# Optimization experiments

Measured on AMD Instinct MI355X. Metric: run time of the kernel, lower is better.

Reference implementation:

```python
import jax, jax.numpy as jnp
import numpy as np

D_MODEL = 256
N_HEADS = 8
N_LEVELS = 4
N_POINTS = 4
D_FFN = 1024
DH = D_MODEL // N_HEADS
SPATIAL = [(100, 100), (50, 50), (25, 25), (13, 13)]  # (H_l, W_l) per level


def setup_inputs() -> dict:
    key = jax.random.key(0)
    ks = iter(jax.random.split(key, 40))
    N, Lq = 8, 900
    Lin = sum(h * w for h, w in SPATIAL)
    p = lambda shape: jax.random.normal(next(ks), shape, jnp.float32) * 0.02
    inp = {
        'idx': 0,
        'tgt': jax.random.normal(next(ks), (N, Lq, D_MODEL), jnp.float32),
        'query_pos': jax.random.normal(next(ks), (N, Lq, D_MODEL), jnp.float32),
        'reference_points_def': jax.random.uniform(next(ks), (N, Lq, N_LEVELS, 2), jnp.float32),
        'src': jax.random.normal(next(ks), (N, Lin, D_MODEL), jnp.float32),
        'src_spatial_shapes': jnp.array(SPATIAL, jnp.int32),
        'level_start_index': jnp.array(np.cumsum([0] + [h * w for h, w in SPATIAL])[:-1], jnp.int32),
        'src_padding_mask': jnp.zeros((N, Lin), bool),
        # self-attn params
        'wq': p((D_MODEL, D_MODEL)), 'bq': jnp.zeros((D_MODEL,)),
        'wk': p((D_MODEL, D_MODEL)), 'bk': jnp.zeros((D_MODEL,)),
        'wv': p((D_MODEL, D_MODEL)), 'bv': jnp.zeros((D_MODEL,)),
        'wo': p((D_MODEL, D_MODEL)), 'bo': jnp.zeros((D_MODEL,)),
        # MSDeformAttn params
        'w_val': p((D_MODEL, D_MODEL)), 'b_val': jnp.zeros((D_MODEL,)),
        'w_off': p((D_MODEL, N_HEADS * N_LEVELS * N_POINTS * 2)), 'b_off': p((N_HEADS * N_LEVELS * N_POINTS * 2,)),
        'w_att': p((D_MODEL, N_HEADS * N_LEVELS * N_POINTS)), 'b_att': jnp.zeros((N_HEADS * N_LEVELS * N_POINTS,)),
        'w_out': p((D_MODEL, D_MODEL)), 'b_out': jnp.zeros((D_MODEL,)),
        # layer norms
        'ln1_g': jnp.ones((D_MODEL,)), 'ln1_b': jnp.zeros((D_MODEL,)),
        'ln2_g': jnp.ones((D_MODEL,)), 'ln2_b': jnp.zeros((D_MODEL,)),
        'ln3_g': jnp.ones((D_MODEL,)), 'ln3_b': jnp.zeros((D_MODEL,)),
        # FFN
        'w1': p((D_MODEL, D_FFN)), 'b1': jnp.zeros((D_FFN,)),
        'w2': p((D_FFN, D_MODEL)), 'b2': jnp.zeros((D_MODEL,)),
    }
    return inp


def _ln(x, g, b):
    m = x.mean(-1, keepdims=True)
    v = jnp.var(x, axis=-1, keepdims=True)
    return (x - m) / jnp.sqrt(v + 1e-5) * g + b


def _mha(q, k, v, wq, bq, wk, bk, wv, bv, wo, bo):
    N, Lq, _ = q.shape
    split = lambda x: x.reshape(N, -1, N_HEADS, DH).transpose(0, 2, 1, 3)  # (N,H,L,dh)
    qh = split(q @ wq + bq) * (1.0 / np.sqrt(DH))
    kh = split(k @ wk + bk)
    vh = split(v @ wv + bv)
    attn = jax.nn.softmax(jnp.einsum('bhqd,bhkd->bhqk', qh, kh), axis=-1)
    o = jnp.einsum('bhqk,bhkd->bhqd', attn, vh).transpose(0, 2, 1, 3).reshape(N, Lq, D_MODEL)
    return o @ wo + bo


def _bilinear(vflat, Hl, Wl, loc):
    # vflat: (N, H, Hl*Wl, dh); loc: (N, Lq, H, P, 2) normalized (x, y) in [0,1]
    N, Lq, _, P, _ = loc.shape
    x = loc[..., 0] * Wl - 0.5  # align_corners=False pixel coords
    y = loc[..., 1] * Hl - 0.5
    x0 = jnp.floor(x); y0 = jnp.floor(y)
    fx = (x - x0).transpose(0, 2, 1, 3).reshape(N, N_HEADS, Lq * P, 1)
    fy = (y - y0).transpose(0, 2, 1, 3).reshape(N, N_HEADS, Lq * P, 1)
    x0i = x0.astype(jnp.int32); y0i = y0.astype(jnp.int32)

    def gather(xi, yi):
        valid = ((xi >= 0) & (xi < Wl) & (yi >= 0) & (yi < Hl)).astype(vflat.dtype)
        idx = jnp.clip(yi, 0, Hl - 1) * Wl + jnp.clip(xi, 0, Wl - 1)
        idx = idx.transpose(0, 2, 1, 3).reshape(N, N_HEADS, Lq * P)
        g = jnp.take_along_axis(vflat, idx[..., None], axis=2)  # (N,H,Lq*P,dh)
        return g * valid.transpose(0, 2, 1, 3).reshape(N, N_HEADS, Lq * P, 1)

    v = (gather(x0i, y0i) * (1 - fx) * (1 - fy)
         + gather(x0i + 1, y0i) * fx * (1 - fy)
         + gather(x0i, y0i + 1) * (1 - fx) * fy
         + gather(x0i + 1, y0i + 1) * fx * fy)
    return v.reshape(N, N_HEADS, Lq, P, DH)


def _msdeform(query, ref, src, ss, pad_mask, w_val, b_val, w_off, b_off, w_att, b_att, w_out, b_out):
    N, Lq, _ = query.shape
    value = src @ w_val + b_val
    value = jnp.where(pad_mask[..., None], 0.0, value)  # masked_fill on padded memory
    off = (query @ w_off + b_off).reshape(N, Lq, N_HEADS, N_LEVELS, N_POINTS, 2)
    att = jax.nn.softmax((query @ w_att + b_att).reshape(N, Lq, N_HEADS, N_LEVELS * N_POINTS), axis=-1)
    att = att.reshape(N, Lq, N_HEADS, N_LEVELS, N_POINTS)
    normalizer = jnp.array([[w, h] for h, w in ss], jnp.float32)  # (L, 2) as (W_l, H_l)
    loc = ref[:, :, None, :, None, :] + off / normalizer[None, None, None, :, None, :]
    out = jnp.zeros((N, N_HEADS, Lq, DH), value.dtype)
    start = 0
    for l, (Hl, Wl) in enumerate(ss):
        vflat = value[:, start:start + Hl * Wl].reshape(N, Hl * Wl, N_HEADS, DH).transpose(0, 2, 1, 3)
        samp = _bilinear(vflat, Hl, Wl, loc[:, :, :, l])  # (N,H,Lq,P,dh)
        w_l = att[:, :, :, l].transpose(0, 2, 1, 3)  # (N,H,Lq,P)
        out = out + (samp * w_l[..., None]).sum(3)
        start += Hl * Wl
    out = out.transpose(0, 2, 1, 3).reshape(N, Lq, D_MODEL)
    return out @ w_out + b_out, loc


def reference(idx, tgt, query_pos, reference_points_def, src, src_spatial_shapes, level_start_index,
              src_padding_mask, wq, bq, wk, bk, wv, bv, wo, bo,
              w_val, b_val, w_off, b_off, w_att, b_att, w_out, b_out,
              ln1_g, ln1_b, ln2_g, ln2_b, ln3_g, ln3_b, w1, b1, w2, b2):
    ss = [tuple(int(v) for v in row) for row in np.asarray(src_spatial_shapes)]
    # self-attention (is_contrastive=False path)
    q = tgt + query_pos
    tgt2 = _mha(q, q, tgt, wq, bq, wk, bk, wv, bv, wo, bo)
    tgt = _ln(tgt + tgt2, ln2_g, ln2_b)
    # multiscale deformable cross-attention
    tgt2, _ = _msdeform(tgt + query_pos, reference_points_def, src, ss, src_padding_mask,
                        w_val, b_val, w_off, b_off, w_att, b_att, w_out, b_out)
    tgt = _ln(tgt + tgt2, ln1_g, ln1_b)
    # FFN
    tgt2 = jax.nn.relu(tgt @ w1 + b1) @ w2 + b2
    tgt = _ln(tgt + tgt2, ln3_g, ln3_b)
    return tgt
```

## Files before the change

kernel.cpp:

```cpp
#include <hip/hip_runtime.h>
#include <math.h>

#define NB 8
#define LQ 900
#define DM 256
#define NH 8
#define DH 32
#define NL 4
#define NP 4
#define DFFN 1024
#define LIN 13294
#define NVAL (NB*LIN)
#define MROW (NB*LQ)
#define GVAL2 3324

#define WP_VAL 0
#define WP_Q   65536
#define WP_K   131072
#define WP_V   196608
#define WP_O   262144
#define WP_OFF 327680
#define WP_ATT 393216
#define WP_OUT 425984
#define WP_W1  491520
#define WP_W2  753664
#define WP_TOT 1015808

typedef __attribute__((ext_vector_type(8))) short bf16x8;
typedef __attribute__((ext_vector_type(4))) float f32x4;

__device__ __forceinline__ unsigned short f2bf(float x) {
  unsigned u = __float_as_uint(x);
  u += 0x7FFFu + ((u >> 16) & 1u);
  return (unsigned short)(u >> 16);
}

__global__ __launch_bounds__(256) void pack_all(
    const float* __restrict__ w_val, const float* __restrict__ wq,
    const float* __restrict__ wk, const float* __restrict__ wv,
    const float* __restrict__ wo, const float* __restrict__ w_off,
    const float* __restrict__ w_att, const float* __restrict__ w_out,
    const float* __restrict__ w1, const float* __restrict__ w2,
    unsigned short* __restrict__ Wp) {
  const int idx = blockIdx.x * 256 + threadIdx.x;
  const float* src; int r, logN;
  if (idx < WP_Q)        { src = w_val; r = idx;          logN = 8; }
  else if (idx < WP_K)   { src = wq;    r = idx - WP_Q;   logN = 8; }
  else if (idx < WP_V)   { src = wk;    r = idx - WP_K;   logN = 8; }
  else if (idx < WP_O)   { src = wv;    r = idx - WP_V;   logN = 8; }
  else if (idx < WP_OFF) { src = wo;    r = idx - WP_O;   logN = 8; }
  else if (idx < WP_ATT) { src = w_off; r = idx - WP_OFF; logN = 8; }
  else if (idx < WP_OUT) { src = w_att; r = idx - WP_ATT; logN = 7; }
  else if (idx < WP_W1)  { src = w_out; r = idx - WP_OUT; logN = 8; }
  else if (idx < WP_W2)  { src = w1;    r = idx - WP_W1;  logN = 10; }
  else                   { src = w2;    r = idx - WP_W2;  logN = 8; }
  const int N = 1 << logN;
  const int e = r & 7, cs = (r >> 3) & 3;
  const int n = (r >> 5) & (N - 1);
  const int kt = r >> (5 + logN);
  const int c = cs ^ ((n >> 1) & 3);
  const int k = kt * 32 + c * 8 + e;
  Wp[idx] = f2bf(src[(size_t)k * N + n]);
}

__global__ __launch_bounds__(256) void value_gemm2(const float* __restrict__ A,
                                                   const unsigned short* __restrict__ Wp,
                                                   const float* __restrict__ bias,
                                                   unsigned short* __restrict__ C,
                                                   int M) {
  __shared__ char lds[17408];
  short* As = (short*)lds;
  short* Bs = (short*)(lds + 4096);
  const int tid = threadIdx.x;
  const int lane = tid & 63, w = tid >> 6;
  const int wr = w >> 1, wc = w & 1;
  const int l15 = lane & 15, lc = lane >> 4;
  const int nwg = gridDim.x;
  const int qq = nwg >> 3, rr = nwg & 7;
  const int xcd = blockIdx.x & 7, pos = blockIdx.x >> 3;
  const int wgid = (xcd < rr ? xcd * (qq + 1) : rr * (qq + 1) + (xcd - rr) * qq) + pos;
  const int m0 = (wgid >> 1) * 64, n0 = (wgid & 1) * 128;
  const int ar = tid >> 2, ac = tid & 3;
  f32x4 acc[2][4] = {};
  for (int kt = 0; kt < 8; kt++) {
    const int arow = min(m0 + ar, M - 1);
    const float* ap = A + (size_t)arow * 256 + kt * 32 + ac * 8;
    const float4 a0 = ((const float4*)ap)[0], a1 = ((const float4*)ap)[1];
    const unsigned short* bp = Wp + ((size_t)(kt * 256 + n0)) * 32 + tid * 16;
    const uint4 b0 = ((const uint4*)bp)[0], b1 = ((const uint4*)bp)[1];
    __syncthreads();
    {
      bf16x8 av;
      av[0] = (short)f2bf(a0.x); av[1] = (short)f2bf(a0.y);
      av[2] = (short)f2bf(a0.z); av[3] = (short)f2bf(a0.w);
      av[4] = (short)f2bf(a1.x); av[5] = (short)f2bf(a1.y);
      av[6] = (short)f2bf(a1.z); av[7] = (short)f2bf(a1.w);
      *(bf16x8*)&As[ar * 32 + ((ac ^ ((ar >> 1) & 3)) << 3)] = av;
      *(uint4*)&Bs[tid * 16] = b0;
      *(uint4*)&Bs[tid * 16 + 8] = b1;
    }
    __syncthreads();
    bf16x8 af[2], bq[4];
#pragma unroll
    for (int i = 0; i < 2; i++) {
      const int row = wr * 32 + i * 16 + l15;
      af[i] = *(const bf16x8*)&As[row * 32 + ((lc ^ ((row >> 1) & 3)) << 3)];
    }
#pragma unroll
    for (int q = 0; q < 4; q++) {
      const int col = wc * 64 + q * 16 + l15;
      bq[q] = *(const bf16x8*)&Bs[col * 32 + ((lc ^ ((col >> 1) & 3)) << 3)];
    }
#pragma unroll
    for (int i = 0; i < 2; i++)
#pragma unroll
      for (int q = 0; q < 4; q++)
        acc[i][q] = __builtin_amdgcn_mfma_f32_16x16x32_bf16(af[i], bq[q], acc[i][q], 0, 0, 0);
  }
  __syncthreads();
  short* strip = (short*)lds + w * 2176;
  float bv[4];
#pragma unroll
  for (int q = 0; q < 4; q++) bv[q] = bias[n0 + wc * 64 + q * 16 + l15];
#pragma unroll
  for (int i = 0; i < 2; i++)
#pragma unroll
    for (int q = 0; q < 4; q++)
#pragma unroll
      for (int r = 0; r < 4; r++)
        strip[(i * 16 + lc * 4 + r) * 68 + q * 16 + l15] = (short)f2bf(acc[i][q][r] + bv[q]);
  __syncthreads();
#pragma unroll
  for (int p = 0; p < 4; p++) {
    const int row = p * 8 + (lane >> 3), c8 = lane & 7;
    const bf16x8 v = *(const bf16x8*)&strip[row * 68 + c8 * 8];
    const int grow = m0 + wr * 32 + row;
    if (grow < M)
      *(bf16x8*)(C + (size_t)grow * 256 + n0 + wc * 64 + c8 * 8) = v;
  }
}

__device__ __forceinline__ void gemm_body(const void* Aptr, const float* A2,
                                          const unsigned short* __restrict__ Wp,
                                          const float* __restrict__ bias, void* Cptr,
                                          int M, int Nn, int K, float scale, int relu,
                                          int a_bf16, int out_bf16, int m0, int n0,
                                          short* As, short* Bs) {
  const int tid = threadIdx.x;
  const int lane = tid & 63, w = tid >> 6;
  const int wr = w >> 1, wc = w & 1;
  const int ar = tid >> 2, ac = tid & 3;
  const int l15 = lane & 15, lc = lane >> 4;
  const int arow = min(m0 + ar, M - 1);
  f32x4 acc[2][2] = {};
  for (int kt = 0; kt < K; kt += 32) {
    bf16x8 av;
    if (a_bf16) {
      av = *(const bf16x8*)((const unsigned short*)Aptr + (size_t)arow * K + kt + ac * 8);
    } else {
      const float* ap = (const float*)Aptr + (size_t)arow * K + kt + ac * 8;
      float4 a0 = ((const float4*)ap)[0], a1 = ((const float4*)ap)[1];
      if (A2) {
        const float* a2p = A2 + (size_t)arow * K + kt + ac * 8;
        const float4 c0 = ((const float4*)a2p)[0], c1 = ((const float4*)a2p)[1];
        a0.x += c0.x; a0.y += c0.y; a0.z += c0.z; a0.w += c0.w;
        a1.x += c1.x; a1.y += c1.y; a1.z += c1.z; a1.w += c1.w;
      }
      av[0] = (short)f2bf(a0.x); av[1] = (short)f2bf(a0.y);
      av[2] = (short)f2bf(a0.z); av[3] = (short)f2bf(a0.w);
      av[4] = (short)f2bf(a1.x); av[5] = (short)f2bf(a1.y);
      av[6] = (short)f2bf(a1.z); av[7] = (short)f2bf(a1.w);
    }
    const unsigned short* bp = Wp + ((size_t)((kt >> 5) * Nn + n0)) * 32 + tid * 8;
    const uint4 b0 = *(const uint4*)bp;
    __syncthreads();
    *(bf16x8*)&As[ar * 32 + ((ac ^ ((ar >> 1) & 3)) << 3)] = av;
    *(uint4*)&Bs[tid * 8] = b0;
    __syncthreads();
    bf16x8 af[2], bf[2];
#pragma unroll
    for (int i = 0; i < 2; i++) {
      const int row = wr * 32 + i * 16 + l15;
      af[i] = *(const bf16x8*)&As[row * 32 + ((lc ^ ((row >> 1) & 3)) << 3)];
      const int col = wc * 32 + i * 16 + l15;
      bf[i] = *(const bf16x8*)&Bs[col * 32 + ((lc ^ ((col >> 1) & 3)) << 3)];
    }
#pragma unroll
    for (int i = 0; i < 2; i++)
#pragma unroll
      for (int j = 0; j < 2; j++)
        acc[i][j] = __builtin_amdgcn_mfma_f32_16x16x32_bf16(af[i], bf[j], acc[i][j], 0, 0, 0);
  }
#pragma unroll
  for (int i = 0; i < 2; i++) {
    const int row0 = m0 + wr * 32 + i * 16 + lc * 4;
#pragma unroll
    for (int j = 0; j < 2; j++) {
      const int col = n0 + wc * 32 + j * 16 + l15;
      const float bv = bias[col];
#pragma unroll
      for (int r = 0; r < 4; r++) {
        const int row = row0 + r;
        if (row < M) {
          float v = (acc[i][j][r] + bv) * scale;
          if (relu) v = fmaxf(v, 0.f);
          if (out_bf16)
            ((unsigned short*)Cptr)[(size_t)row * Nn + col] = f2bf(v);
          else
            ((float*)Cptr)[(size_t)row * Nn + col] = v;
        }
      }
    }
  }
}

__global__ __launch_bounds__(256) void gemm_qkv(const float* __restrict__ tgt,
                                                const float* __restrict__ qpos,
                                                const unsigned short* __restrict__ Wp,
                                                const float* __restrict__ bq_,
                                                const float* __restrict__ bk_,
                                                const float* __restrict__ bv_,
                                                unsigned short* Qb, unsigned short* Kb,
                                                unsigned short* Vb, float qscale) {
  __shared__ short As[64 * 32];
  __shared__ short Bs[64 * 32];
  const int z = blockIdx.z;
  const unsigned short* W = Wp + (z == 0 ? WP_Q : z == 1 ? WP_K : WP_V);
  const float* bias = (z == 0) ? bq_ : (z == 1) ? bk_ : bv_;
  unsigned short* C = (z == 0) ? Qb : (z == 1) ? Kb : Vb;
  const float* A2 = (z == 2) ? nullptr : qpos;
  gemm_body(tgt, A2, W, bias, C, MROW, DM, DM, (z == 0) ? qscale : 1.f, 0, 0, 1,
            blockIdx.y * 64, blockIdx.x * 64, As, Bs);
}

__global__ __launch_bounds__(256) void gemm_offatt(const float* __restrict__ x1,
                                                   const float* __restrict__ qpos,
                                                   const unsigned short* __restrict__ Wp,
                                                   const float* __restrict__ b_off,
                                                   const float* __restrict__ b_att,
                                                   float* offb, float* attb) {
  const int z = blockIdx.z;
  if (z == 1 && blockIdx.x >= 2) return;
  __shared__ short As[64 * 32];
  __shared__ short Bs[64 * 32];
  const unsigned short* W = Wp + (z ? WP_ATT : WP_OFF);
  const float* bias = z ? b_att : b_off;
  float* C = z ? attb : offb;
  const int Nn = z ? 128 : 256;
  gemm_body(x1, qpos, W, bias, C, MROW, Nn, DM, 1.f, 0, 0, 0,
            blockIdx.y * 64, blockIdx.x * 64, As, Bs);
}

__global__ __launch_bounds__(256) void gemm_fused(const void* A, const unsigned short* Wp,
                                                  const float* bias, void* C, int M, int Nn,
                                                  int K, float scale, int relu, int a_bf16,
                                                  int out_bf16) {
  __shared__ short As[64 * 32];
  __shared__ short Bs[64 * 32];
  gemm_body(A, nullptr, Wp, bias, C, M, Nn, K, scale, relu, a_bf16, out_bf16,
            blockIdx.y * 64, blockIdx.x * 64, As, Bs);
}

__global__ __launch_bounds__(256) void attn_mfma(const unsigned short* __restrict__ Qg,
                                                 const unsigned short* __restrict__ Kg,
                                                 const unsigned short* __restrict__ Vg,
                                                 unsigned short* __restrict__ O) {
  __shared__ short Ks[2048];
  __shared__ short Vt[2048];
  __shared__ short Pl[4096];
  const int tid = threadIdx.x;
  const int lane = tid & 63, w = tid >> 6;
  const int l15 = lane & 15, lc = lane >> 4;
  const int h = blockIdx.y, b = blockIdx.z;
  const int q0 = blockIdx.x * 64;
  char* KsB = (char*)Ks; char* VtB = (char*)Vt; char* PlB = (char*)Pl + w * 2048;

  bf16x8 qa;
  {
    const int qrow = min(q0 + w * 16 + l15, LQ - 1);
    qa = *(const bf16x8*)(Qg + ((size_t)(b * LQ + qrow)) * DM + h * DH + lc * 8);
  }
  f32x4 o0 = {0.f, 0.f, 0.f, 0.f}, o1 = {0.f, 0.f, 0.f, 0.f};
  float mrow[4], lrow[4];
#pragma unroll
  for (int r = 0; r < 4; r++) { mrow[r] = -1e30f; lrow[r] = 0.f; }
  const int skey = tid >> 2, sq = tid & 3;

  for (int kt = 0; kt < LQ; kt += 64) {
    const int kr = min(kt + skey, LQ - 1);
    const bf16x8 kb = *(const bf16x8*)(Kg + ((size_t)(b * LQ + kr)) * DM + h * DH + sq * 8);
    const bf16x8 vv = *(const bf16x8*)(Vg + ((size_t)(b * LQ + kr)) * DM + h * DH + sq * 8);
    __syncthreads();
    {
      *(bf16x8*)(KsB + ((skey * 64 + sq * 16) ^ ((skey & 7) << 4))) = kb;
#pragma unroll
      for (int j = 0; j < 8; j++) {
        const int dh = sq * 8 + j;
        const int qz = ((dh & 7) ^ (((dh >> 3) & 3) << 1)) << 4;
        *(short*)(VtB + ((dh * 128 + skey * 2) ^ qz)) = (short)vv[j];
      }
    }
    __syncthreads();
    f32x4 s[4];
#pragma unroll
    for (int cb = 0; cb < 4; cb++) {
      const int key = cb * 16 + l15;
      const bf16x8 kf = *(const bf16x8*)(KsB + ((key * 64 + lc * 16) ^ ((key & 7) << 4)));
      const f32x4 z = {0.f, 0.f, 0.f, 0.f};
      s[cb] = __builtin_amdgcn_mfma_f32_16x16x32_bf16(qa, kf, z, 0, 0, 0);
    }
#pragma unroll
    for (int cb = 0; cb < 4; cb++)
      if (kt + cb * 16 + l15 >= LQ) {
        s[cb][0] = -1e30f; s[cb][1] = -1e30f; s[cb][2] = -1e30f; s[cb][3] = -1e30f;
      }
    float tm[4], fs[4], ps[4];
#pragma unroll
    for (int r = 0; r < 4; r++)
      tm[r] = fmaxf(fmaxf(s[0][r], s[1][r]), fmaxf(s[2][r], s[3][r]));
#pragma unroll
    for (int msk = 1; msk <= 8; msk <<= 1)
#pragma unroll
      for (int r = 0; r < 4; r++) tm[r] = fmaxf(tm[r], __shfl_xor(tm[r], msk));
#pragma unroll
    for (int r = 0; r < 4; r++) {
      const float nm = fmaxf(mrow[r], tm[r]);
      fs[r] = __expf(mrow[r] - nm);
      mrow[r] = nm;
    }
#pragma unroll
    for (int cb = 0; cb < 4; cb++)
#pragma unroll
      for (int r = 0; r < 4; r++) s[cb][r] = __expf(s[cb][r] - mrow[r]);
#pragma unroll
    for (int r = 0; r < 4; r++) ps[r] = (s[0][r] + s[1][r]) + (s[2][r] + s[3][r]);
#pragma unroll
    for (int msk = 1; msk <= 8; msk <<= 1)
#pragma unroll
      for (int r = 0; r < 4; r++) ps[r] += __shfl_xor(ps[r], msk);
#pragma unroll
    for (int r = 0; r < 4; r++) {
      lrow[r] = lrow[r] * fs[r] + ps[r];
      o0[r] *= fs[r]; o1[r] *= fs[r];
    }
#pragma unroll
    for (int cb = 0; cb < 4; cb++)
#pragma unroll
      for (int r = 0; r < 4; r++) {
        const int row = lc * 4 + r, col = cb * 16 + l15;
        *(short*)(PlB + ((row * 128 + col * 2) ^ ((row & 7) << 4))) = (short)f2bf(s[cb][r]);
      }
#pragma unroll
    for (int ks2 = 0; ks2 < 2; ks2++) {
      const int koff2 = (ks2 * 32 + lc * 8) * 2;
      const bf16x8 pa = *(const bf16x8*)(PlB + ((l15 * 128 + koff2) ^ ((l15 & 7) << 4)));
      {
        const int dh = l15;
        const int qz = ((dh & 7) ^ (((dh >> 3) & 3) << 1)) << 4;
        const bf16x8 vf = *(const bf16x8*)(VtB + ((dh * 128 + koff2) ^ qz));
        o0 = __builtin_amdgcn_mfma_f32_16x16x32_bf16(pa, vf, o0, 0, 0, 0);
      }
      {
        const int dh = 16 + l15;
        const int qz = ((dh & 7) ^ (((dh >> 3) & 3) << 1)) << 4;
        const bf16x8 vf = *(const bf16x8*)(VtB + ((dh * 128 + koff2) ^ qz));
        o1 = __builtin_amdgcn_mfma_f32_16x16x32_bf16(pa, vf, o1, 0, 0, 0);
      }
    }
  }
#pragma unroll
  for (int r = 0; r < 4; r++) {
    const int qrow = q0 + w * 16 + lc * 4 + r;
    if (qrow < LQ) {
      const float inv = 1.f / lrow[r];
      unsigned short* op = O + ((size_t)(b * LQ + qrow)) * DM + h * DH;
      op[l15] = f2bf(o0[r] * inv);
      op[16 + l15] = f2bf(o1[r] * inv);
    }
  }
}

__global__ __launch_bounds__(256) void sample_kernel(const unsigned short* __restrict__ value,
                                                     const float* __restrict__ ref,
                                                     const float* __restrict__ off,
                                                     const float* __restrict__ att,
                                                     unsigned short* __restrict__ out) {
  const int t = blockIdx.x * 256 + threadIdx.x;
  const int d8 = t & 3;
  const int h = (t >> 2) & 7;
  const int qb = t >> 5;
  const int b = qb / LQ;
  const int HLs[4] = {100, 50, 25, 13};
  const int STs[4] = {0, 10000, 12500, 13125};
  const float* rp = ref + (size_t)qb * (NL * 2);
  const float* op = off + (size_t)qb * DM + h * (NL * NP * 2);
  const float* ap = att + (size_t)qb * (NH * NL * NP) + h * (NL * NP);
  const unsigned short* vb = value + (size_t)b * LIN * DM + h * DH + d8 * 8;

  float aw[16];
#pragma unroll
  for (int i = 0; i < 4; i++) {
    const float4 a4 = ((const float4*)ap)[i];
    aw[4 * i] = a4.x; aw[4 * i + 1] = a4.y; aw[4 * i + 2] = a4.z; aw[4 * i + 3] = a4.w;
  }
  float am = aw[0];
#pragma unroll
  for (int i = 1; i < 16; i++) am = fmaxf(am, aw[i]);
  float asum = 0.f;
#pragma unroll
  for (int i = 0; i < 16; i++) { aw[i] = __expf(aw[i] - am); asum += aw[i]; }
  const float ainv = 1.f / asum;

  float acc[8] = {};
#pragma unroll
  for (int l = 0; l < NL; l++) {
    const int Hl = HLs[l], Wl = HLs[l], st = STs[l];
    const float rx = rp[l * 2], ry = rp[l * 2 + 1];
#pragma unroll
    for (int p = 0; p < NP; p++) {
      const float2 o2 = ((const float2*)op)[l * NP + p];
      const float a = aw[l * NP + p] * ainv;
      const float locx = rx + o2.x / (float)Wl;
      const float locy = ry + o2.y / (float)Hl;
      const float x = locx * (float)Wl - 0.5f;
      const float y = locy * (float)Hl - 0.5f;
      const float xf = floorf(x), yf = floorf(y);
      const float fx = x - xf, fy = y - yf;
      const int x0 = (int)xf, y0 = (int)yf;
      const int x1 = x0 + 1, y1 = y0 + 1;
      const float vx0 = (x0 >= 0 && x0 < Wl) ? 1.f : 0.f;
      const float vx1 = (x1 >= 0 && x1 < Wl) ? 1.f : 0.f;
      const float vy0 = (y0 >= 0 && y0 < Hl) ? 1.f : 0.f;
      const float vy1 = (y1 >= 0 && y1 < Hl) ? 1.f : 0.f;
      const int cx0 = min(max(x0, 0), Wl - 1), cx1 = min(max(x1, 0), Wl - 1);
      const int cy0 = min(max(y0, 0), Hl - 1), cy1 = min(max(y1, 0), Hl - 1);
      const float w00 = a * (1.f - fx) * (1.f - fy) * vx0 * vy0;
      const float w10 = a * fx * (1.f - fy) * vx1 * vy0;
      const float w01 = a * (1.f - fx) * fy * vx0 * vy1;
      const float w11 = a * fx * fy * vx1 * vy1;
      const unsigned short* r0 = vb + (size_t)(st + cy0 * Wl) * DM;
      const unsigned short* r1 = vb + (size_t)(st + cy1 * Wl) * DM;
      const uint4 g00 = *(const uint4*)(r0 + (size_t)cx0 * DM);
      const uint4 g10 = *(const uint4*)(r0 + (size_t)cx1 * DM);
      const uint4 g01 = *(const uint4*)(r1 + (size_t)cx0 * DM);
      const uint4 g11 = *(const uint4*)(r1 + (size_t)cx1 * DM);
      const unsigned u00[4] = {g00.x, g00.y, g00.z, g00.w};
      const unsigned u10[4] = {g10.x, g10.y, g10.z, g10.w};
      const unsigned u01[4] = {g01.x, g01.y, g01.z, g01.w};
      const unsigned u11[4] = {g11.x, g11.y, g11.z, g11.w};
#pragma unroll
      for (int i = 0; i < 4; i++) {
        acc[2 * i]     += w00 * __uint_as_float(u00[i] << 16) + w10 * __uint_as_float(u10[i] << 16)
                        + w01 * __uint_as_float(u01[i] << 16) + w11 * __uint_as_float(u11[i] << 16);
        acc[2 * i + 1] += w00 * __uint_as_float(u00[i] & 0xFFFF0000u) + w10 * __uint_as_float(u10[i] & 0xFFFF0000u)
                        + w01 * __uint_as_float(u01[i] & 0xFFFF0000u) + w11 * __uint_as_float(u11[i] & 0xFFFF0000u);
      }
    }
  }
  bf16x8 ov;
#pragma unroll
  for (int i = 0; i < 8; i++) ov[i] = (short)f2bf(acc[i]);
  *(bf16x8*)(out + (size_t)t * 8) = ov;
}

__global__ __launch_bounds__(256) void ln_kernel(const float* __restrict__ A,
                                                 const float* __restrict__ R,
                                                 const float* __restrict__ g,
                                                 const float* __restrict__ be,
                                                 float* __restrict__ out) {
  const int row = blockIdx.x * 4 + (threadIdx.x >> 6);
  const int t = threadIdx.x & 63;
  const float4 va = ((const float4*)(A + (size_t)row * DM))[t];
  const float4 vr = ((const float4*)(R + (size_t)row * DM))[t];
  const float x0 = va.x + vr.x, x1 = va.y + vr.y, x2 = va.z + vr.z, x3 = va.w + vr.w;
  float s = x0 + x1 + x2 + x3;
  float ss = x0 * x0 + x1 * x1 + x2 * x2 + x3 * x3;
#pragma unroll
  for (int o = 1; o < 64; o <<= 1) { s += __shfl_xor(s, o); ss += __shfl_xor(ss, o); }
  const float mean = s * (1.f / DM);
  const float var = ss * (1.f / DM) - mean * mean;
  const float rstd = rsqrtf(var + 1e-5f);
  const float4 vg = ((const float4*)g)[t];
  const float4 vb = ((const float4*)be)[t];
  float4 o4;
  o4.x = (x0 - mean) * rstd * vg.x + vb.x;
  o4.y = (x1 - mean) * rstd * vg.y + vb.y;
  o4.z = (x2 - mean) * rstd * vg.z + vb.z;
  o4.w = (x3 - mean) * rstd * vg.w + vb.w;
  ((float4*)(out + (size_t)row * DM))[t] = o4;
}

extern "C" void kernel_launch(void* const* d_in, const int* in_sizes, int n_in,
                              void* d_out, int out_size, void* d_ws, size_t ws_size,
                              hipStream_t stream) {
  const float* tgt  = (const float*)d_in[1];
  const float* qpos = (const float*)d_in[2];
  const float* ref  = (const float*)d_in[3];
  const float* src  = (const float*)d_in[4];
  const float* wq = (const float*)d_in[8];  const float* bq = (const float*)d_in[9];
  const float* wk = (const float*)d_in[10]; const float* bk = (const float*)d_in[11];
  const float* wv = (const float*)d_in[12]; const float* bv = (const float*)d_in[13];
  const float* wo = (const float*)d_in[14]; const float* bo = (const float*)d_in[15];
  const float* w_val = (const float*)d_in[16]; const float* b_val = (const float*)d_in[17];
  const float* w_off = (const float*)d_in[18]; const float* b_off = (const float*)d_in[19];
  const float* w_att = (const float*)d_in[20]; const float* b_att = (const float*)d_in[21];
  const float* w_out = (const float*)d_in[22]; const float* b_out = (const float*)d_in[23];
  const float* ln1g = (const float*)d_in[24]; const float* ln1b = (const float*)d_in[25];
  const float* ln2g = (const float*)d_in[26]; const float* ln2b = (const float*)d_in[27];
  const float* ln3g = (const float*)d_in[28]; const float* ln3b = (const float*)d_in[29];
  const float* w1 = (const float*)d_in[30]; const float* b1 = (const float*)d_in[31];
  const float* w2 = (const float*)d_in[32]; const float* b2 = (const float*)d_in[33];

  const size_t S = (size_t)MROW * DM;
  const size_t VAL_F = (size_t)NVAL * DM;
  float* ws = (float*)d_ws;
  float* value = ws;
  unsigned short* wp = (unsigned short*)(ws + VAL_F / 2);
  float* B0   = ws + VAL_F;
  unsigned short* Qb = (unsigned short*)(B0 + 1 * S);
  unsigned short* Kb = (unsigned short*)(B0 + 2 * S);
  unsigned short* Vb = (unsigned short*)(B0 + 3 * S);
  unsigned short* Ob = (unsigned short*)(B0 + 4 * S);
  float* tmp  = B0 + 5 * S;
  float* x1   = B0 + 0 * S;
  float* offb = B0 + 2 * S;
  float* attb = B0 + 3 * S;
  unsigned short* samp = (unsigned short*)(B0 + 4 * S);
  float* x2   = B0 + 6 * S;
  unsigned short* hffn = (unsigned short*)(B0 + 1 * S);

  const float qscale = 0.17677669529663687f;
  const dim3 blk(256);
  const dim3 gQ(DM / 64, (MROW + 63) / 64);

  pack_all<<<dim3(WP_TOT / 256), blk, 0, stream>>>(w_val, wq, wk, wv, wo, w_off, w_att,
                                                   w_out, w1, w2, wp);

  gemm_qkv<<<dim3(4, 113, 3), blk, 0, stream>>>(tgt, qpos, wp, bq, bk, bv,
                                                Qb, Kb, Vb, qscale);
  attn_mfma<<<dim3((LQ + 63) / 64, NH, NB), blk, 0, stream>>>(Qb, Kb, Vb, Ob);
  gemm_fused<<<gQ, blk, 0, stream>>>(Ob, wp + WP_O, bo, tmp, MROW, DM, DM, 1.f, 0, 1, 0);
  ln_kernel<<<dim3(MROW / 4), blk, 0, stream>>>(tmp, tgt, ln2g, ln2b, x1);

  value_gemm2<<<dim3(GVAL2), blk, 0, stream>>>(src, wp + WP_VAL, b_val,
                                               (unsigned short*)value, NVAL);
  gemm_offatt<<<dim3(4, 113, 2), blk, 0, stream>>>(x1, qpos, wp, b_off, b_att, offb, attb);
  sample_kernel<<<dim3((MROW * NH * 4) / 256), blk, 0, stream>>>(
      (const unsigned short*)value, ref, offb, attb, samp);
  gemm_fused<<<gQ, blk, 0, stream>>>(samp, wp + WP_OUT, b_out, tmp, MROW, DM, DM,
                                     1.f, 0, 1, 0);
  ln_kernel<<<dim3(MROW / 4), blk, 0, stream>>>(tmp, x1, ln1g, ln1b, x2);

  gemm_fused<<<dim3(DFFN / 64, 113), blk, 0, stream>>>(x2, wp + WP_W1, b1, hffn, MROW,
                                                       DFFN, DM, 1.f, 1, 0, 1);
  gemm_fused<<<gQ, blk, 0, stream>>>(hffn, wp + WP_W2, b2, tmp, MROW, DM, DFFN,
                                     1.f, 0, 1, 0);
  ln_kernel<<<dim3(MROW / 4), blk, 0, stream>>>(tmp, x2, ln3g, ln3b, (float*)d_out);
}
```

Measured before the change: 256.8 us.

## Restructure value GEMM into independent per-wave tiles without block barriers

Rewrites the value projection GEMM so each wave independently computes a 32x64 output tile. Each wave stages its own A strip in a double-buffered private LDS region and loads B fragments straight from the pre-packed global weights, which removes every block-wide __syncthreads from the K loop and the epilogue. The block tile becomes 128x64 instead of 64x128, so each A row is fetched by four column tiles instead of two. That extra A traffic is expected to be absorbed by L2 because adjacent tiles map to the same XCD, and B is re-read from cache by every wave.

```diff
diff --git a/kernel.cpp b/kernel.cpp
--- a/kernel.cpp
+++ b/kernel.cpp
@@ -12,7 +12,7 @@
 #define LIN 13294
 #define NVAL (NB*LIN)
 #define MROW (NB*LQ)
-#define GVAL2 3324
+#define GVAL3 3324
 
 #define WP_VAL 0
 #define WP_Q   65536
@@ -63,53 +63,56 @@
   Wp[idx] = f2bf(src[(size_t)k * N + n]);
 }
 
-__global__ __launch_bounds__(256) void value_gemm2(const float* __restrict__ A,
+__global__ __launch_bounds__(256) void value_gemm3(const float* __restrict__ A,
                                                    const unsigned short* __restrict__ Wp,
                                                    const float* __restrict__ bias,
                                                    unsigned short* __restrict__ C,
                                                    int M) {
-  __shared__ char lds[17408];
-  short* As = (short*)lds;
-  short* Bs = (short*)(lds + 4096);
+  __shared__ short lds[4][2048];
   const int tid = threadIdx.x;
   const int lane = tid & 63, w = tid >> 6;
-  const int wr = w >> 1, wc = w & 1;
   const int l15 = lane & 15, lc = lane >> 4;
   const int nwg = gridDim.x;
   const int qq = nwg >> 3, rr = nwg & 7;
   const int xcd = blockIdx.x & 7, pos = blockIdx.x >> 3;
   const int wgid = (xcd < rr ? xcd * (qq + 1) : rr * (qq + 1) + (xcd - rr) * qq) + pos;
-  const int m0 = (wgid >> 1) * 64, n0 = (wgid & 1) * 128;
-  const int ar = tid >> 2, ac = tid & 3;
+  const int mt = wgid >> 2, nt = wgid & 3;
+  const int m0 = mt * 128 + w * 32;
+  const int n0 = nt * 64;
+  const int sr = lane >> 1, kh = lane & 1;
+  short* strips = lds[w];
+  const int arow = min(m0 + sr, M - 1);
   f32x4 acc[2][4] = {};
+#pragma unroll
   for (int kt = 0; kt < 8; kt++) {
-    const int arow = min(m0 + ar, M - 1);
-    const float* ap = A + (size_t)arow * 256 + kt * 32 + ac * 8;
+    const float* ap = A + (size_t)arow * 256 + kt * 32 + kh * 16;
     const float4 a0 = ((const float4*)ap)[0], a1 = ((const float4*)ap)[1];
-    const unsigned short* bp = Wp + ((size_t)(kt * 256 + n0)) * 32 + tid * 16;
-    const uint4 b0 = ((const uint4*)bp)[0], b1 = ((const uint4*)bp)[1];
-    __syncthreads();
-    {
-      bf16x8 av;
-      av[0] = (short)f2bf(a0.x); av[1] = (short)f2bf(a0.y);
-      av[2] = (short)f2bf(a0.z); av[3] = (short)f2bf(a0.w);
-      av[4] = (short)f2bf(a1.x); av[5] = (short)f2bf(a1.y);
-      av[6] = (short)f2bf(a1.z); av[7] = (short)f2bf(a1.w);
-      *(bf16x8*)&As[ar * 32 + ((ac ^ ((ar >> 1) & 3)) << 3)] = av;
-      *(uint4*)&Bs[tid * 16] = b0;
-      *(uint4*)&Bs[tid * 16 + 8] = b1;
-    }
-    __syncthreads();
-    bf16x8 af[2], bq[4];
+    const float4 a2 = ((const float4*)ap)[2], a3 = ((const float4*)ap)[3];
+    bf16x8 bq[4];
+#pragma unroll
+    for (int q = 0; q < 4; q++) {
+      const int col = n0 + q * 16 + l15;
+      bq[q] = *(const bf16x8*)(Wp + ((size_t)(kt * 256 + col)) * 32 +
+                               ((lc ^ ((col >> 1) & 3)) << 3));
+    }
+    short* st = strips + (kt & 1) * 1024;
+    bf16x8 av0, av1;
+    av0[0] = (short)f2bf(a0.x); av0[1] = (short)f2bf(a0.y);
+    av0[2] = (short)f2bf(a0.z); av0[3] = (short)f2bf(a0.w);
+    av0[4] = (short)f2bf(a1.x); av0[5] = (short)f2bf(a1.y);
+    av0[6] = (short)f2bf(a1.z); av0[7] = (short)f2bf(a1.w);
+    av1[0] = (short)f2bf(a2.x); av1[1] = (short)f2bf(a2.y);
+    av1[2] = (short)f2bf(a2.z); av1[3] = (short)f2bf(a2.w);
+    av1[4] = (short)f2bf(a3.x); av1[5] = (short)f2bf(a3.y);
+    av1[6] = (short)f2bf(a3.z); av1[7] = (short)f2bf(a3.w);
+    const int c0 = kh * 2, c1 = c0 + 1;
+    *(bf16x8*)&st[sr * 32 + ((c0 ^ (sr & 3)) << 3)] = av0;
+    *(bf16x8*)&st[sr * 32 + ((c1 ^ (sr & 3)) << 3)] = av1;
+    bf16x8 af[2];
 #pragma unroll
     for (int i = 0; i < 2; i++) {
-      const int row = wr * 32 + i * 16 + l15;
-      af[i] = *(const bf16x8*)&As[row * 32 + ((lc ^ ((row >> 1) & 3)) << 3)];
-    }
-#pragma unroll
-    for (int q = 0; q < 4; q++) {
-      const int col = wc * 64 + q * 16 + l15;
-      bq[q] = *(const bf16x8*)&Bs[col * 32 + ((lc ^ ((col >> 1) & 3)) << 3)];
+      const int row = i * 16 + l15;
+      af[i] = *(const bf16x8*)&st[row * 32 + ((lc ^ (row & 3)) << 3)];
     }
 #pragma unroll
     for (int i = 0; i < 2; i++)
@@ -117,26 +120,23 @@
       for (int q = 0; q < 4; q++)
         acc[i][q] = __builtin_amdgcn_mfma_f32_16x16x32_bf16(af[i], bq[q], acc[i][q], 0, 0, 0);
   }
-  __syncthreads();
-  short* strip = (short*)lds + w * 2176;
   float bv[4];
 #pragma unroll
-  for (int q = 0; q < 4; q++) bv[q] = bias[n0 + wc * 64 + q * 16 + l15];
+  for (int q = 0; q < 4; q++) bv[q] = bias[n0 + q * 16 + l15];
 #pragma unroll
   for (int i = 0; i < 2; i++)
 #pragma unroll
     for (int q = 0; q < 4; q++)
 #pragma unroll
       for (int r = 0; r < 4; r++)
-        strip[(i * 16 + lc * 4 + r) * 68 + q * 16 + l15] = (short)f2bf(acc[i][q][r] + bv[q]);
-  __syncthreads();
-#pragma unroll
-  for (int p = 0; p < 4; p++) {
-    const int row = p * 8 + (lane >> 3), c8 = lane & 7;
-    const bf16x8 v = *(const bf16x8*)&strip[row * 68 + c8 * 8];
-    const int grow = m0 + wr * 32 + row;
-    if (grow < M)
-      *(bf16x8*)(C + (size_t)grow * 256 + n0 + wc * 64 + c8 * 8) = v;
+        strips[(i * 16 + lc * 4 + r) * 64 + q * 16 + l15] = (short)f2bf(acc[i][q][r] + bv[q]);
+  const int grow = m0 + sr;
+  if (grow < M) {
+#pragma unroll
+    for (int j = 0; j < 4; j++) {
+      const bf16x8 v = *(const bf16x8*)&strips[sr * 64 + kh * 32 + j * 8];
+      *(bf16x8*)(C + (size_t)grow * 256 + n0 + kh * 32 + j * 8) = v;
+    }
   }
 }
 
@@ -542,7 +542,7 @@
   gemm_fused<<<gQ, blk, 0, stream>>>(Ob, wp + WP_O, bo, tmp, MROW, DM, DM, 1.f, 0, 1, 0);
   ln_kernel<<<dim3(MROW / 4), blk, 0, stream>>>(tmp, tgt, ln2g, ln2b, x1);
 
-  value_gemm2<<<dim3(GVAL2), blk, 0, stream>>>(src, wp + WP_VAL, b_val,
+  value_gemm3<<<dim3(GVAL3), blk, 0, stream>>>(src, wp + WP_VAL, b_val,
                                                (unsigned short*)value, NVAL);
   gemm_offatt<<<dim3(4, 113, 2), blk, 0, stream>>>(x1, qpos, wp, b_off, b_att, offb, attb);
   sample_kernel<<<dim3((MROW * NH * 4) / 256), blk, 0, stream>>>(
```

New measurement: 280.4 us. 1.09x slower.

## Double-buffer LDS tiles and prefetch next K-slice in GEMM kernels

Applied to the files above, without the earlier changes.

Both the value projection GEMM and the generic gemm_body now keep two LDS buffers and issue the global loads for the next K tile before the MFMA work on the current one. This drops one of the two barriers per K step and hides global load latency behind compute. The cost is more LDS per block, which may reduce occupancy, and more registers held for the prefetched data.

```diff
diff --git a/kernel.cpp b/kernel.cpp
--- a/kernel.cpp
+++ b/kernel.cpp
@@ -63,14 +63,14 @@
   Wp[idx] = f2bf(src[(size_t)k * N + n]);
 }
 
-__global__ __launch_bounds__(256) void value_gemm2(const float* __restrict__ A,
+__global__ __launch_bounds__(256) void value_gemm4(const float* __restrict__ A,
                                                    const unsigned short* __restrict__ Wp,
                                                    const float* __restrict__ bias,
                                                    unsigned short* __restrict__ C,
                                                    int M) {
-  __shared__ char lds[17408];
+  __shared__ char lds[24576];
   short* As = (short*)lds;
-  short* Bs = (short*)(lds + 4096);
+  short* Bs = (short*)(lds + 8192);
   const int tid = threadIdx.x;
   const int lane = tid & 63, w = tid >> 6;
   const int wr = w >> 1, wc = w & 1;
@@ -81,35 +81,46 @@
   const int wgid = (xcd < rr ? xcd * (qq + 1) : rr * (qq + 1) + (xcd - rr) * qq) + pos;
   const int m0 = (wgid >> 1) * 64, n0 = (wgid & 1) * 128;
   const int ar = tid >> 2, ac = tid & 3;
+  const int arow = min(m0 + ar, M - 1);
   f32x4 acc[2][4] = {};
-  for (int kt = 0; kt < 8; kt++) {
-    const int arow = min(m0 + ar, M - 1);
-    const float* ap = A + (size_t)arow * 256 + kt * 32 + ac * 8;
-    const float4 a0 = ((const float4*)ap)[0], a1 = ((const float4*)ap)[1];
-    const unsigned short* bp = Wp + ((size_t)(kt * 256 + n0)) * 32 + tid * 16;
-    const uint4 b0 = ((const uint4*)bp)[0], b1 = ((const uint4*)bp)[1];
-    __syncthreads();
+  float4 pa0, pa1; uint4 pb0, pb1;
+  {
+    const float* ap_ = A + (size_t)arow * 256 + ac * 8;
+    pa0 = ((const float4*)ap_)[0]; pa1 = ((const float4*)ap_)[1];
+    const unsigned short* bp_ = Wp + ((size_t)n0) * 32 + tid * 16;
+    pb0 = ((const uint4*)bp_)[0]; pb1 = ((const uint4*)bp_)[1];
+  }
+#pragma unroll
+  for (int kt = 0; kt < 256; kt += 32) {
+    short* Ac = As + ((kt >> 5) & 1) * 2048;
+    short* Bc = Bs + ((kt >> 5) & 1) * 4096;
     {
       bf16x8 av;
-      av[0] = (short)f2bf(a0.x); av[1] = (short)f2bf(a0.y);
-      av[2] = (short)f2bf(a0.z); av[3] = (short)f2bf(a0.w);
-      av[4] = (short)f2bf(a1.x); av[5] = (short)f2bf(a1.y);
-      av[6] = (short)f2bf(a1.z); av[7] = (short)f2bf(a1.w);
-      *(bf16x8*)&As[ar * 32 + ((ac ^ ((ar >> 1) & 3)) << 3)] = av;
-      *(uint4*)&Bs[tid * 16] = b0;
-      *(uint4*)&Bs[tid * 16 + 8] = b1;
+      av[0] = (short)f2bf(pa0.x); av[1] = (short)f2bf(pa0.y);
+      av[2] = (short)f2bf(pa0.z); av[3] = (short)f2bf(pa0.w);
+      av[4] = (short)f2bf(pa1.x); av[5] = (short)f2bf(pa1.y);
+      av[6] = (short)f2bf(pa1.z); av[7] = (short)f2bf(pa1.w);
+      *(bf16x8*)&Ac[ar * 32 + ((ac ^ ((ar >> 1) & 3)) << 3)] = av;
+      *(uint4*)&Bc[tid * 16] = pb0;
+      *(uint4*)&Bc[tid * 16 + 8] = pb1;
     }
     __syncthreads();
+    if (kt + 32 < 256) {
+      const float* ap_ = A + (size_t)arow * 256 + kt + 32 + ac * 8;
+      pa0 = ((const float4*)ap_)[0]; pa1 = ((const float4*)ap_)[1];
+      const unsigned short* bp_ = Wp + ((size_t)(((kt >> 5) + 1) * 256 + n0)) * 32 + tid * 16;
+      pb0 = ((const uint4*)bp_)[0]; pb1 = ((const uint4*)bp_)[1];
+    }
     bf16x8 af[2], bq[4];
 #pragma unroll
     for (int i = 0; i < 2; i++) {
       const int row = wr * 32 + i * 16 + l15;
-      af[i] = *(const bf16x8*)&As[row * 32 + ((lc ^ ((row >> 1) & 3)) << 3)];
+      af[i] = *(const bf16x8*)&Ac[row * 32 + ((lc ^ ((row >> 1) & 3)) << 3)];
     }
 #pragma unroll
     for (int q = 0; q < 4; q++) {
       const int col = wc * 64 + q * 16 + l15;
-      bq[q] = *(const bf16x8*)&Bs[col * 32 + ((lc ^ ((col >> 1) & 3)) << 3)];
+      bq[q] = *(const bf16x8*)&Bc[col * 32 + ((lc ^ ((col >> 1) & 3)) << 3)];
     }
 #pragma unroll
     for (int i = 0; i < 2; i++)
@@ -153,37 +164,62 @@
   const int l15 = lane & 15, lc = lane >> 4;
   const int arow = min(m0 + ar, M - 1);
   f32x4 acc[2][2] = {};
+  float4 pa0, pa1, pc0, pc1; bf16x8 pav; uint4 pb;
+  {
+    if (a_bf16) {
+      pav = *(const bf16x8*)((const unsigned short*)Aptr + (size_t)arow * K + ac * 8);
+    } else {
+      const float* ap_ = (const float*)Aptr + (size_t)arow * K + ac * 8;
+      pa0 = ((const float4*)ap_)[0]; pa1 = ((const float4*)ap_)[1];
+      if (A2) {
+        const float* cp_ = A2 + (size_t)arow * K + ac * 8;
+        pc0 = ((const float4*)cp_)[0]; pc1 = ((const float4*)cp_)[1];
+      }
+    }
+    pb = *(const uint4*)(Wp + ((size_t)n0) * 32 + tid * 8);
+  }
   for (int kt = 0; kt < K; kt += 32) {
-    bf16x8 av;
-    if (a_bf16) {
-      av = *(const bf16x8*)((const unsigned short*)Aptr + (size_t)arow * K + kt + ac * 8);
-    } else {
-      const float* ap = (const float*)Aptr + (size_t)arow * K + kt + ac * 8;
-      float4 a0 = ((const float4*)ap)[0], a1 = ((const float4*)ap)[1];
-      if (A2) {
-        const float* a2p = A2 + (size_t)arow * K + kt + ac * 8;
-        const float4 c0 = ((const float4*)a2p)[0], c1 = ((const float4*)a2p)[1];
-        a0.x += c0.x; a0.y += c0.y; a0.z += c0.z; a0.w += c0.w;
-        a1.x += c1.x; a1.y += c1.y; a1.z += c1.z; a1.w += c1.w;
-      }
-      av[0] = (short)f2bf(a0.x); av[1] = (short)f2bf(a0.y);
-      av[2] = (short)f2bf(a0.z); av[3] = (short)f2bf(a0.w);
-      av[4] = (short)f2bf(a1.x); av[5] = (short)f2bf(a1.y);
-      av[6] = (short)f2bf(a1.z); av[7] = (short)f2bf(a1.w);
-    }
-    const unsigned short* bp = Wp + ((size_t)((kt >> 5) * Nn + n0)) * 32 + tid * 8;
-    const uint4 b0 = *(const uint4*)bp;
+    short* Ac = As + ((kt >> 5) & 1) * 2048;
+    short* Bc = Bs + ((kt >> 5) & 1) * 2048;
+    {
+      bf16x8 av;
+      if (a_bf16) {
+        av = pav;
+      } else {
+        float4 a0 = pa0, a1 = pa1;
+        if (A2) {
+          a0.x += pc0.x; a0.y += pc0.y; a0.z += pc0.z; a0.w += pc0.w;
+          a1.x += pc1.x; a1.y += pc1.y; a1.z += pc1.z; a1.w += pc1.w;
+        }
+        av[0] = (short)f2bf(a0.x); av[1] = (short)f2bf(a0.y);
+        av[2] = (short)f2bf(a0.z); av[3] = (short)f2bf(a0.w);
+        av[4] = (short)f2bf(a1.x); av[5] = (short)f2bf(a1.y);
+        av[6] = (short)f2bf(a1.z); av[7] = (short)f2bf(a1.w);
+      }
+      *(bf16x8*)&Ac[ar * 32 + ((ac ^ ((ar >> 1) & 3)) << 3)] = av;
+      *(uint4*)&Bc[tid * 8] = pb;
+    }
     __syncthreads();
-    *(bf16x8*)&As[ar * 32 + ((ac ^ ((ar >> 1) & 3)) << 3)] = av;
-    *(uint4*)&Bs[tid * 8] = b0;
-    __syncthreads();
+    if (kt + 32 < K) {
+      if (a_bf16) {
+        pav = *(const bf16x8*)((const unsigned short*)Aptr + (size_t)arow * K + kt + 32 + ac * 8);
+      } else {
+        const float* ap_ = (const float*)Aptr + (size_t)arow * K + kt + 32 + ac * 8;
+        pa0 = ((const float4*)ap_)[0]; pa1 = ((const float4*)ap_)[1];
+        if (A2) {
+          const float* cp_ = A2 + (size_t)arow * K + kt + 32 + ac * 8;
+          pc0 = ((const float4*)cp_)[0]; pc1 = ((const float4*)cp_)[1];
+        }
+      }
+      pb = *(const uint4*)(Wp + ((size_t)(((kt >> 5) + 1) * Nn + n0)) * 32 + tid * 8);
+    }
     bf16x8 af[2], bf[2];
 #pragma unroll
     for (int i = 0; i < 2; i++) {
       const int row = wr * 32 + i * 16 + l15;
-      af[i] = *(const bf16x8*)&As[row * 32 + ((lc ^ ((row >> 1) & 3)) << 3)];
+      af[i] = *(const bf16x8*)&Ac[row * 32 + ((lc ^ ((row >> 1) & 3)) << 3)];
       const int col = wc * 32 + i * 16 + l15;
-      bf[i] = *(const bf16x8*)&Bs[col * 32 + ((lc ^ ((col >> 1) & 3)) << 3)];
+      bf[i] = *(const bf16x8*)&Bc[col * 32 + ((lc ^ ((col >> 1) & 3)) << 3)];
     }
 #pragma unroll
     for (int i = 0; i < 2; i++)
@@ -222,8 +258,8 @@
                                                 const float* __restrict__ bv_,
                                                 unsigned short* Qb, unsigned short* Kb,
                                                 unsigned short* Vb, float qscale) {
-  __shared__ short As[64 * 32];
-  __shared__ short Bs[64 * 32];
+  __shared__ short As[2 * 2048];
+  __shared__ short Bs[2 * 2048];
   const int z = blockIdx.z;
   const unsigned short* W = Wp + (z == 0 ? WP_Q : z == 1 ? WP_K : WP_V);
   const float* bias = (z == 0) ? bq_ : (z == 1) ? bk_ : bv_;
@@ -241,8 +277,8 @@
                                                    float* offb, float* attb) {
   const int z = blockIdx.z;
   if (z == 1 && blockIdx.x >= 2) return;
-  __shared__ short As[64 * 32];
-  __shared__ short Bs[64 * 32];
+  __shared__ short As[2 * 2048];
+  __shared__ short Bs[2 * 2048];
   const unsigned short* W = Wp + (z ? WP_ATT : WP_OFF);
   const float* bias = z ? b_att : b_off;
   float* C = z ? attb : offb;
@@ -255,8 +291,8 @@
                                                   const float* bias, void* C, int M, int Nn,
                                                   int K, float scale, int relu, int a_bf16,
                                                   int out_bf16) {
-  __shared__ short As[64 * 32];
-  __shared__ short Bs[64 * 32];
+  __shared__ short As[2 * 2048];
+  __shared__ short Bs[2 * 2048];
   gemm_body(A, nullptr, Wp, bias, C, M, Nn, K, scale, relu, a_bf16, out_bf16,
             blockIdx.y * 64, blockIdx.x * 64, As, Bs);
 }
@@ -542,7 +578,7 @@
   gemm_fused<<<gQ, blk, 0, stream>>>(Ob, wp + WP_O, bo, tmp, MROW, DM, DM, 1.f, 0, 1, 0);
   ln_kernel<<<dim3(MROW / 4), blk, 0, stream>>>(tmp, tgt, ln2g, ln2b, x1);
 
-  value_gemm2<<<dim3(GVAL2), blk, 0, stream>>>(src, wp + WP_VAL, b_val,
+  value_gemm4<<<dim3(GVAL2), blk, 0, stream>>>(src, wp + WP_VAL, b_val,
                                                (unsigned short*)value, NVAL);
   gemm_offatt<<<dim3(4, 113, 2), blk, 0, stream>>>(x1, qpos, wp, b_off, b_att, offb, attb);
   sample_kernel<<<dim3((MROW * NH * 4) / 256), blk, 0, stream>>>(
```

Result: no change. 258.7 us (+0.8%).
